# Kernel tuning notes

Measured on AMD Instinct MI355X. Metric: run time of the kernel, lower is better.

Reference implementation:

```python
import jax, jax.numpy as jnp
import numpy as np

NUM_LAYERS = 32
NUM_SLOTS = 128
HIDDEN = 4096
T_WRITE = 128   # == NUM_SLOTS so slot_ids form a permutation (deterministic scatter)
T_READ = 8192
EMA_ALPHA = 0.1


def setup_inputs() -> dict:
    key = jax.random.key(0)
    ks = jax.random.split(key, 4)
    values = jax.random.normal(ks[0], (T_WRITE, HIDDEN), jnp.float32)
    queries = jax.random.normal(ks[1], (T_READ, HIDDEN), jnp.float32)
    memory = jax.random.normal(ks[2], (NUM_LAYERS, NUM_SLOTS, HIDDEN), jnp.float32) * 0.02
    gate_w = jax.random.normal(ks[3], (NUM_LAYERS, HIDDEN), jnp.float32) * (1.0 / np.sqrt(HIDDEN))
    gate_b = jnp.zeros((NUM_LAYERS,), jnp.float32)
    return {
        "values": values,
        "queries": queries,
        "memory": memory,
        "gate_w": gate_w,
        "gate_b": gate_b,
        "layer_idx": 0,
        "k": 8,
        "ptr": 0,
    }


def reference(values, queries, memory, gate_w, gate_b, layer_idx, k, ptr):
    # ---- write(): EMA scatter into one layer's slots ----
    mem_l = memory[layer_idx]                                  # [N, d]
    g = jax.nn.sigmoid(values @ gate_w[layer_idx] + gate_b[layer_idx])[:, None]  # [T,1]
    T = values.shape[0]
    slot_ids = (ptr + jnp.arange(T)) % NUM_SLOTS               # [T]
    current = mem_l[slot_ids]                                  # gather [T, d]
    updated = EMA_ALPHA * g * values + (1.0 - EMA_ALPHA) * current
    mem_new = mem_l.at[slot_ids].set(updated)                  # scatter-write [N, d]

    # ---- read(): matmul -> top-k -> gather -> softmax -> weighted sum ----
    scale = 1.0 / jnp.sqrt(jnp.float32(HIDDEN))
    scores = (queries @ mem_new.T) * scale                     # [T_read, N]
    topk_scores, topk_idx = jax.lax.top_k(scores, k)           # [T_read, k]
    attn = jax.nn.softmax(topk_scores, axis=-1)                # [T_read, k]
    topk_v = mem_new[topk_idx]                                 # gather [T_read, k, d]
    out = jnp.einsum('tk,tkd->td', attn, topk_v)               # [T_read, d]
    return out
```

## Files before the change

### kernel.cpp

```cpp
#include <hip/hip_runtime.h>
#include <math.h>

#define D 4096
#define NSLOTS 128
#define TR 8192
#define NKQ 8
#define KCH 512
#define EPS_TRIG 1e-3f
#define WIN 5e-4f

typedef __attribute__((ext_vector_type(8))) short bf16x8;
typedef __attribute__((ext_vector_type(4))) float f32x4;

union BV { bf16x8 v; unsigned u[4]; };

__device__ __forceinline__ unsigned short bfrne(float x) {
  unsigned u = __float_as_uint(x);
  unsigned r = u + 0x7fffu + ((u >> 16) & 1u);
  return (unsigned short)(r >> 16);
}

__device__ __forceinline__ void gload16(const void* gsrc, void* ldst) {
  __builtin_amdgcn_global_load_lds(
      (const __attribute__((address_space(1))) void*)gsrc,
      (__attribute__((address_space(3))) void*)ldst, 16, 0, 0);
}

__global__ __launch_bounds__(256) void update_mem_kernel(
    const float* __restrict__ values, const float* __restrict__ memory,
    const float* __restrict__ gate_w, const float* __restrict__ gate_b,
    const int* __restrict__ layer_idx_p, const int* __restrict__ ptr_p,
    int T_W, float* __restrict__ ws_mem,
    unsigned short* __restrict__ MFh,
    unsigned short* __restrict__ BTFh, unsigned short* __restrict__ BTFm) {
  const int l = layer_idx_p[0], p = ptr_p[0], s = blockIdx.x, tid = threadIdx.x;
  int t0 = ((s - p) % NSLOTS + NSLOTS) % NSLOTS;
  const bool written = (t0 < T_W);
  const int t = written ? (t0 + ((T_W - 1 - t0) / NSLOTS) * NSLOTS) : 0;
  const float* mrow = memory + ((size_t)l * NSLOTS + s) * D;
  const float* vrow = values + (size_t)t * D;

  float acoef = 0.f, bcoef = 1.0f;
  if (written) {
    const float* gw = gate_w + (size_t)l * D;
    double acc = 0.0;
    for (int j = tid; j < D; j += 256)
      acc += (double)vrow[j] * (double)gw[j];
    for (int off = 32; off; off >>= 1) acc += __shfl_down(acc, off, 64);
    __shared__ double wsum[4];
    if ((tid & 63) == 0) wsum[tid >> 6] = acc;
    __syncthreads();
    double dot = wsum[0] + wsum[1] + wsum[2] + wsum[3];
    float x = (float)dot + gate_b[l];
    float g = 1.0f / (1.0f + expf(-x));
    acoef = 0.1f * g; bcoef = 0.9f;
  }

  const int sg = s >> 4, fr_s = s & 15;
  const int ksS = s >> 5, foS = (s >> 3) & 3, posS = s & 7;
  for (int j8 = tid; j8 < D / 8; j8 += 256) {
    float4 mv0 = ((const float4*)mrow)[j8 * 2];
    float4 mv1 = ((const float4*)mrow)[j8 * 2 + 1];
    float4 vv0 = make_float4(0.f, 0.f, 0.f, 0.f), vv1 = vv0;
    if (written) {
      vv0 = ((const float4*)vrow)[j8 * 2];
      vv1 = ((const float4*)vrow)[j8 * 2 + 1];
    }
    float ov[8];
    ov[0] = acoef * vv0.x + bcoef * mv0.x;
    ov[1] = acoef * vv0.y + bcoef * mv0.y;
    ov[2] = acoef * vv0.z + bcoef * mv0.z;
    ov[3] = acoef * vv0.w + bcoef * mv0.w;
    ov[4] = acoef * vv1.x + bcoef * mv1.x;
    ov[5] = acoef * vv1.y + bcoef * mv1.y;
    ov[6] = acoef * vv1.z + bcoef * mv1.z;
    ov[7] = acoef * vv1.w + bcoef * mv1.w;
    ((float4*)(ws_mem + (size_t)s * D))[j8 * 2] =
        make_float4(ov[0], ov[1], ov[2], ov[3]);
    ((float4*)(ws_mem + (size_t)s * D))[j8 * 2 + 1] =
        make_float4(ov[4], ov[5], ov[6], ov[7]);

    unsigned short h[8], md[8];
#pragma unroll
    for (int e = 0; e < 8; ++e) {
      h[e] = bfrne(ov[e]);
      float f = __uint_as_float((unsigned)h[e] << 16);
      md[e] = bfrne(ov[e] - f);
    }
    const int ks = j8 >> 2, fo = j8 & 3;
    const size_t unit = (size_t)ks * 512 + sg * 64 + fo * 16 + fr_s;
    uint4 hp;
    hp.x = (unsigned)h[0] | ((unsigned)h[1] << 16);
    hp.y = (unsigned)h[2] | ((unsigned)h[3] << 16);
    hp.z = (unsigned)h[4] | ((unsigned)h[5] << 16);
    hp.w = (unsigned)h[6] | ((unsigned)h[7] << 16);
    ((uint4*)MFh)[unit] = hp;
#pragma unroll
    for (int e = 0; e < 8; ++e) {
      int c = j8 * 8 + e;
      size_t u = ((size_t)(c >> 4) * 4 + ksS) * 64 + foS * 16 + (c & 15);
      BTFh[u * 8 + posS] = h[e];
      BTFm[u * 8 + posS] = md[e];
    }
  }
}

__global__ __launch_bounds__(256, 4) void scores_kernel(
    const float* __restrict__ queries, const unsigned short* __restrict__ MFh,
    float* __restrict__ part) {
  __shared__ float Qs[2][2048];

  const int tid = threadIdx.x, lane = tid & 63, w = tid >> 6;
  const int fr = lane & 15, fo = lane >> 4;
  const int qt = blockIdx.x >> 3, kq = blockIdx.x & (NKQ - 1);
  const int qbase = qt * 64;
  const int kbase = kq * KCH;

  const int rl = lane >> 3, ul = lane & 7;
  const int su = ul ^ rl;
  const float* qsrc[2];
#pragma unroll
  for (int i = 0; i < 2; ++i) {
    int g = w * 2 + i;
    qsrc[i] = queries + (size_t)(qbase + 8 * g + rl) * D + kbase + su * 4;
  }

  const unsigned short* bh_base = MFh + (size_t)lane * 8;
  const size_t kqoff = (size_t)kq * 16 * 512 * 8;

  f32x4 acc[8];
#pragma unroll
  for (int cg = 0; cg < 8; ++cg) acc[cg] = (f32x4){0.f, 0.f, 0.f, 0.f};

  const int rowA = w * 16 + fr;

#define STG(B, S) do {                                                       \
    const int k0_ = (S) * 32;                                                \
    _Pragma("unroll")                                                        \
    for (int i = 0; i < 2; ++i)                                              \
      gload16(qsrc[i] + k0_, &Qs[B][(w * 2 + i) * 256]);                     \
  } while (0)

#define CMP(B, S) do {                                                       \
    const size_t soff = kqoff + (size_t)(S) * 512 * 8;                       \
    bf16x8 bh_[8];                                                           \
    _Pragma("unroll")                                                        \
    for (int cg = 0; cg < 8; ++cg)                                           \
      bh_[cg] = *(const bf16x8*)(bh_base + soff + cg * 64 * 8);              \
    float4 a0 = *(const float4*)&Qs[B][rowA * 32 + (((fo * 2) ^ (rowA & 7)) << 2)]; \
    float4 a1 = *(const float4*)&Qs[B][rowA * 32 + ((((fo * 2) | 1) ^ (rowA & 7)) << 2)]; \
    float qf[8] = {a0.x, a0.y, a0.z, a0.w, a1.x, a1.y, a1.z, a1.w};          \
    BV ah;                                                                   \
    _Pragma("unroll")                                                        \
    for (int i = 0; i < 4; ++i) {                                            \
      unsigned u0 = __float_as_uint(qf[2 * i]);                              \
      unsigned u1 = __float_as_uint(qf[2 * i + 1]);                          \
      ah.u[i] = (u0 >> 16) | (u1 & 0xffff0000u);           \
    }                                                                        \
    _Pragma("unroll")                                                        \
    for (int cg = 0; cg < 8; ++cg)                                           \
      acc[cg] = __builtin_amdgcn_mfma_f32_16x16x32_bf16(ah.v, bh_[cg], acc[cg], 0, 0, 0); \
  } while (0)

  STG(0, 0);
  __syncthreads();
  for (int s = 0; s < 16; ++s) {
    const int cur = s & 1;
    if (s < 15) STG(cur ^ 1, s + 1);
    CMP(cur, s);
    __syncthreads();
  }
#undef STG
#undef CMP

  float* op = part + ((size_t)kq * TR + qbase) * NSLOTS;
#pragma unroll
  for (int cg = 0; cg < 8; ++cg)
#pragma unroll
    for (int r = 0; r < 4; ++r)
      op[(size_t)(w * 16 + fo * 4 + r) * NSLOTS + cg * 16 + fr] = acc[cg][r];
}

__device__ __forceinline__ unsigned mapf(float f) {
  unsigned u = __float_as_uint(f);
  return (u & 0x80000000u) ? ~u : (u | 0x80000000u);
}
__device__ __forceinline__ float unmapf(unsigned u) {
  return __uint_as_float((u & 0x80000000u) ? (u & 0x7fffffffu) : ~u);
}

__device__ __forceinline__ void wave_select(
    float va, float vb, int l, int k, int iters,
    float &m, float &sum, bool &sela, bool &selb, float &vkm1, float &vkk) {
  m = 0.f; sum = 0.f; sela = false; selb = false; vkm1 = 0.f; vkk = -3.4e38f;
  for (int it = 0; it < iters; ++it) {
    unsigned long long ka =
        ((unsigned long long)mapf(va) << 32) | (unsigned)(127 - l);
    unsigned long long kb =
        ((unsigned long long)mapf(vb) << 32) | (unsigned)(63 - l);
    unsigned long long key = ka > kb ? ka : kb;
#pragma unroll
    for (int off = 32; off; off >>= 1) {
      unsigned long long o = __shfl_xor(key, off, 64);
      if (o > key) key = o;
    }
    int idx = 127 - (int)(unsigned)(key & 0xffffffffULL);
    float val = unmapf((unsigned)(key >> 32));
    if (it == 0) m = val;
    if (it < k) sum += expf(val - m);
    if (it == k - 1) vkm1 = val;
    if (it == k) vkk = val;
    if (idx == l) { sela = sela || (it < k); va = -INFINITY; }
    if (idx == l + 64) { selb = selb || (it < k); vb = -INFINITY; }
  }
}

__device__ __forceinline__ float rescore_slot(const float* __restrict__ qrow,
                                              const float* __restrict__ mrow,
                                              int l) {
  double acc = 0.0;
#pragma unroll 4
  for (int c = 0; c < 16; ++c) {
    int j = c * 256 + l * 4;
    float4 qv = *(const float4*)(qrow + j);
    float4 mv = *(const float4*)(mrow + j);
    acc += (double)qv.x * (double)mv.x;
    acc += (double)qv.y * (double)mv.y;
    acc += (double)qv.z * (double)mv.z;
    acc += (double)qv.w * (double)mv.w;
  }
#pragma unroll
  for (int off = 32; off; off >>= 1) acc += __shfl_xor(acc, off, 64);
  return (float)(acc * 0.015625);
}

__global__ __launch_bounds__(256) void topk_kernel(
    const float* __restrict__ part, const float* __restrict__ ws_mem,
    const float* __restrict__ queries, const int* __restrict__ k_p,
    unsigned short* __restrict__ AFh, unsigned short* __restrict__ AFm) {
  const int w = threadIdx.x >> 6, l = threadIdx.x & 63;
  const int row = blockIdx.x * 4 + w;
  int k = k_p[0];
  if (k < 1) k = 1;
  if (k > NSLOTS) k = NSLOTS;
  const int ksel = (k < NSLOTS) ? k + 1 : k;

  float origa = 0.f, origb = 0.f;
#pragma unroll
  for (int kq = 0; kq < NKQ; ++kq) {
    origa += part[((size_t)kq * TR + row) * NSLOTS + l];
    origb += part[((size_t)kq * TR + row) * NSLOTS + 64 + l];
  }
  origa *= 0.015625f;
  origb *= 0.015625f;

  float m, sum, vkm1, vkk;
  bool sela, selb;
  wave_select(origa, origb, l, k, ksel, m, sum, sela, selb, vkm1, vkk);

  if (ksel > k && (vkm1 - vkk) < EPS_TRIG) {
    const float* qrow = queries + (size_t)row * D;
    float lo = vkk - WIN, hi = vkm1 + WIN;
    unsigned long long ba = __ballot(origa >= lo && origa <= hi);
    unsigned long long bb = __ballot(origb >= lo && origb <= hi);
    while (ba) {
      int s = __ffsll(ba) - 1; ba &= ba - 1;
      float ex = rescore_slot(qrow, ws_mem + (size_t)s * D, l);
      if (l == s) origa = ex;
    }
    while (bb) {
      int s = __ffsll(bb) - 1; bb &= bb - 1;
      float ex = rescore_slot(qrow, ws_mem + (size_t)(s + 64) * D, l);
      if (l == s) origb = ex;
    }
    wave_select(origa, origb, l, k, k, m, sum, sela, selb, vkm1, vkk);
  }

  const float inv = 1.0f / sum;
  float wa = sela ? expf(origa - m) * inv : 0.f;
  float wb = selb ? expf(origb - m) * inv : 0.f;

  unsigned short ha = bfrne(wa);
  unsigned short ma = bfrne(wa - __uint_as_float((unsigned)ha << 16));
  unsigned short hb = bfrne(wb);
  unsigned short mb = bfrne(wb - __uint_as_float((unsigned)hb << 16));

  const int rg = row >> 4, frr = row & 15;
  const size_t ua =
      (((size_t)rg * 4 + (l >> 5)) * 64 + ((l >> 3) & 3) * 16 + frr) * 8 + (l & 7);
  const size_t ub =
      (((size_t)rg * 4 + (l >> 5) + 2) * 64 + ((l >> 3) & 3) * 16 + frr) * 8 + (l & 7);
  AFh[ua] = ha; AFm[ua] = ma;
  AFh[ub] = hb; AFm[ub] = mb;
}

__global__ __launch_bounds__(256) void gather_kernel(
    const unsigned short* __restrict__ AFh, const unsigned short* __restrict__ AFm,
    const unsigned short* __restrict__ BTFh, const unsigned short* __restrict__ BTFm,
    float* __restrict__ out) {
  const int tid = threadIdx.x, lane = tid & 63, w = tid >> 6;
  const int fr = lane & 15, fo = lane >> 4;
  const int rowblk = blockIdx.x >> 5, colblk = blockIdx.x & 31;
  const int r0 = rowblk * 128 + w * 32;
  const int rg0 = r0 >> 4;

  bf16x8 a_h[2][4], a_m[2][4];
#pragma unroll
  for (int rg = 0; rg < 2; ++rg)
#pragma unroll
    for (int ks = 0; ks < 4; ++ks) {
      const size_t u = (((size_t)(rg0 + rg) * 4 + ks) * 64 + lane) * 8;
      a_h[rg][ks] = *(const bf16x8*)(AFh + u);
      a_m[rg][ks] = *(const bf16x8*)(AFm + u);
    }

#pragma unroll 2
  for (int cgi = 0; cgi < 8; ++cgi) {
    const int cg = colblk * 8 + cgi;
    bf16x8 b_h[4], b_m[4];
#pragma unroll
    for (int ks = 0; ks < 4; ++ks) {
      const size_t u = (((size_t)cg * 4 + ks) * 64 + lane) * 8;
      b_h[ks] = *(const bf16x8*)(BTFh + u);
      b_m[ks] = *(const bf16x8*)(BTFm + u);
    }
    const int col = cg * 16 + fr;
#pragma unroll
    for (int rg = 0; rg < 2; ++rg) {
      f32x4 acc = {0.f, 0.f, 0.f, 0.f};
#pragma unroll
      for (int ks = 0; ks < 4; ++ks) {
        acc = __builtin_amdgcn_mfma_f32_16x16x32_bf16(a_m[rg][ks], b_h[ks], acc, 0, 0, 0);
        acc = __builtin_amdgcn_mfma_f32_16x16x32_bf16(a_h[rg][ks], b_m[ks], acc, 0, 0, 0);
        acc = __builtin_amdgcn_mfma_f32_16x16x32_bf16(a_h[rg][ks], b_h[ks], acc, 0, 0, 0);
      }
#pragma unroll
      for (int r = 0; r < 4; ++r)
        out[(size_t)(r0 + rg * 16 + fo * 4 + r) * D + col] = acc[r];
    }
  }
}

extern "C" void kernel_launch(void* const* d_in, const int* in_sizes, int n_in,
                              void* d_out, int out_size, void* d_ws, size_t ws_size,
                              hipStream_t stream) {
  const float* values  = (const float*)d_in[0];
  const float* queries = (const float*)d_in[1];
  const float* memory  = (const float*)d_in[2];
  const float* gate_w  = (const float*)d_in[3];
  const float* gate_b  = (const float*)d_in[4];
  const int* layer_idx = (const int*)d_in[5];
  const int* k_p       = (const int*)d_in[6];
  const int* ptr_p     = (const int*)d_in[7];

  const int T_W = in_sizes[0] / D;
  const int T_R = in_sizes[1] / D;

  float* ws_mem = (float*)d_ws;
  float* part   = ws_mem + (size_t)NSLOTS * D;
  unsigned short* MFh  = (unsigned short*)(part + (size_t)NKQ * TR * NSLOTS);
  unsigned short* BTFh = MFh  + (size_t)NSLOTS * D;
  unsigned short* BTFm = BTFh + (size_t)NSLOTS * D;
  unsigned short* AFh  = BTFm + (size_t)NSLOTS * D;
  unsigned short* AFm  = AFh  + (size_t)T_R * NSLOTS;

  update_mem_kernel<<<NSLOTS, 256, 0, stream>>>(
      values, memory, gate_w, gate_b, layer_idx, ptr_p, T_W,
      ws_mem, MFh, BTFh, BTFm);
  scores_kernel<<<(T_R / 64) * NKQ, 256, 0, stream>>>(queries, MFh, part);
  topk_kernel<<<T_R / 4, 256, 0, stream>>>(part, ws_mem, queries, k_p, AFh, AFm);
  gather_kernel<<<(T_R / 128) * (D / 128), 256, 0, stream>>>(AFh, AFm, BTFh, BTFm,
                                                             (float*)d_out);
}
```

Measured before the change: 162.5 us.

## Stage B fragments through LDS with a 4-buffer, depth-2 async prefetch pipeline

The scores kernel now copies the bf16 memory fragments into LDS with async global_load_lds, alongside the query tiles, instead of loading them straight from global memory into registers inside the compute step. Buffering grows from 2 to 4 stages with a prefetch distance of 2. Explicit vmcnt waits and a single barrier per step replace the two __syncthreads per iteration. The aim is to hide global-load latency for both operands and cut sync overhead, at the cost of more LDS per block and dropping the occupancy hint in launch_bounds.

```diff
diff --git a/kernel.cpp b/kernel.cpp
--- a/kernel.cpp
+++ b/kernel.cpp
@@ -105,10 +105,11 @@
   }
 }
 
-__global__ __launch_bounds__(256, 4) void scores_kernel(
+__global__ __launch_bounds__(256) void scores_kernel(
     const float* __restrict__ queries, const unsigned short* __restrict__ MFh,
     float* __restrict__ part) {
-  __shared__ float Qs[2][2048];
+  __shared__ float Qs[4][2048];
+  __shared__ unsigned short Bs[4][4096];
 
   const int tid = threadIdx.x, lane = tid & 63, w = tid >> 6;
   const int fr = lane & 15, fo = lane >> 4;
@@ -121,12 +122,10 @@
   const float* qsrc[2];
 #pragma unroll
   for (int i = 0; i < 2; ++i) {
-    int g = w * 2 + i;
-    qsrc[i] = queries + (size_t)(qbase + 8 * g + rl) * D + kbase + su * 4;
-  }
-
-  const unsigned short* bh_base = MFh + (size_t)lane * 8;
-  const size_t kqoff = (size_t)kq * 16 * 512 * 8;
+    int dl = w * 2 + i;
+    qsrc[i] = queries + (size_t)(qbase + 8 * dl + rl) * D + kbase + su * 4;
+  }
+  const unsigned short* bsrc = MFh + (size_t)kq * 16 * 4096 + (size_t)lane * 8;
 
   f32x4 acc[8];
 #pragma unroll
@@ -134,21 +133,24 @@
 
   const int rowA = w * 16 + fr;
 
-#define STG(B, S) do {                                                       \
-    const int k0_ = (S) * 32;                                                \
+#define STG(B_, S_) do {                                                     \
+    const int k0_ = (S_) * 32;                                               \
     _Pragma("unroll")                                                        \
     for (int i = 0; i < 2; ++i)                                              \
-      gload16(qsrc[i] + k0_, &Qs[B][(w * 2 + i) * 256]);                     \
+      gload16(qsrc[i] + k0_, &Qs[B_][(w * 2 + i) * 256]);                    \
+    _Pragma("unroll")                                                        \
+    for (int i = 0; i < 2; ++i)                                              \
+      gload16(bsrc + (size_t)(S_) * 4096 + (w * 2 + i) * 512,                \
+              &Bs[B_][(w * 2 + i) * 512]);                                   \
   } while (0)
 
-#define CMP(B, S) do {                                                       \
-    const size_t soff = kqoff + (size_t)(S) * 512 * 8;                       \
+#define CMP(B_) do {                                                         \
     bf16x8 bh_[8];                                                           \
     _Pragma("unroll")                                                        \
     for (int cg = 0; cg < 8; ++cg)                                           \
-      bh_[cg] = *(const bf16x8*)(bh_base + soff + cg * 64 * 8);              \
-    float4 a0 = *(const float4*)&Qs[B][rowA * 32 + (((fo * 2) ^ (rowA & 7)) << 2)]; \
-    float4 a1 = *(const float4*)&Qs[B][rowA * 32 + ((((fo * 2) | 1) ^ (rowA & 7)) << 2)]; \
+      bh_[cg] = *(const bf16x8*)&Bs[B_][(cg * 64 + lane) * 8];               \
+    float4 a0 = *(const float4*)&Qs[B_][rowA * 32 + (((fo * 2) ^ (rowA & 7)) << 2)]; \
+    float4 a1 = *(const float4*)&Qs[B_][rowA * 32 + ((((fo * 2) | 1) ^ (rowA & 7)) << 2)]; \
     float qf[8] = {a0.x, a0.y, a0.z, a0.w, a1.x, a1.y, a1.z, a1.w};          \
     BV ah;                                                                   \
     _Pragma("unroll")                                                        \
@@ -163,12 +165,16 @@
   } while (0)
 
   STG(0, 0);
-  __syncthreads();
+  STG(1, 1);
+#pragma unroll
   for (int s = 0; s < 16; ++s) {
-    const int cur = s & 1;
-    if (s < 15) STG(cur ^ 1, s + 1);
-    CMP(cur, s);
-    __syncthreads();
+    if (s + 2 < 16) STG((s + 2) & 3, s + 2);
+    if (s <= 13)      asm volatile("s_waitcnt vmcnt(8)" ::: "memory");
+    else if (s == 14) asm volatile("s_waitcnt vmcnt(4)" ::: "memory");
+    else              asm volatile("s_waitcnt vmcnt(0)" ::: "memory");
+    __builtin_amdgcn_sched_barrier(0);
+    __builtin_amdgcn_s_barrier();
+    CMP(s & 3);
   }
 #undef STG
 #undef CMP
```

Result: faster. 132.5 us (-18.5%).
